# Performance work log

Hardware: AMD Instinct MI355X
Metric: run time of the kernel (lower is better)

Reference implementation:

```python
import jax, jax.numpy as jnp
import numpy as np
import jax.scipy.linalg as jsl

N = 20000
E = 320000
IN_FEAT = 128
HID = 128
OUT_FEAT = 64
D = 4            # stalk_dim
K = HID // D     # number of stalks per node
MLP_HID = 64


def setup_inputs() -> dict:
    key = jax.random.key(0)
    ks = jax.random.split(key, 16)
    def lin(kw, kb, fan_in, fan_out):
        s = 1.0 / np.sqrt(fan_in)
        w = jax.random.uniform(kw, (fan_in, fan_out), minval=-s, maxval=s, dtype=jnp.float32)
        b = jax.random.uniform(kb, (fan_out,), minval=-s, maxval=s, dtype=jnp.float32)
        return w, b
    x = jax.random.normal(ks[0], (N, IN_FEAT), dtype=jnp.float32)
    edge_index = jax.random.randint(ks[1], (2, E), 0, N, dtype=jnp.int64)
    lin_in_w, lin_in_b = lin(ks[2], ks[3], IN_FEAT, HID)
    conv0_w1, conv0_b1 = lin(ks[4], ks[5], 2 * HID, MLP_HID)
    conv0_w2, conv0_b2 = lin(ks[6], ks[7], MLP_HID, 2 * D * D)
    conv1_w1, conv1_b1 = lin(ks[8], ks[9], 2 * HID, MLP_HID)
    conv1_w2, conv1_b2 = lin(ks[10], ks[11], MLP_HID, 2 * D * D)
    lin_out_w, lin_out_b = lin(ks[12], ks[13], HID, OUT_FEAT)
    return {
        "x": x, "edge_index": edge_index,
        "lin_in_w": lin_in_w, "lin_in_b": lin_in_b,
        "conv0_w1": conv0_w1, "conv0_b1": conv0_b1,
        "conv0_w2": conv0_w2, "conv0_b2": conv0_b2, "conv0_eps": jnp.float32(0.5),
        "conv1_w1": conv1_w1, "conv1_b1": conv1_b1,
        "conv1_w2": conv1_w2, "conv1_b2": conv1_b2, "conv1_eps": jnp.float32(0.5),
        "lin_out_w": lin_out_w, "lin_out_b": lin_out_b,
    }


def _sheaf_conv(x, row, col, w1, b1, w2, b2, eps):
    # edge gather -> MLP -> skew-symmetric expm -> batched small matmuls -> scatter-add
    x_row = x[row]              # [E, C] source features
    x_col = x[col]              # [E, C] target features
    h = jax.nn.relu(jnp.concatenate([x_row, x_col], axis=-1) @ w1 + b1)
    maps = (h @ w2 + b2).reshape(-1, 2, D, D)        # [E, 2, d, d]
    A = maps - jnp.swapaxes(maps, -1, -2)            # skew-symmetric
    F_e = jax.vmap(jsl.expm)(A.reshape(-1, D, D)).reshape(-1, 2, D, D)
    f_u, f_v = F_e[:, 0], F_e[:, 1]                  # [E, d, d] each
    # PyG default flow: x_i = x[col] (target), x_j = x[row] (source)
    x_i = x_col.reshape(-1, K, D)
    x_j = x_row.reshape(-1, K, D)
    proj_i = jnp.einsum('eab,ekb->eka', f_u, x_i)
    proj_j = jnp.einsum('eab,ekb->eka', f_v, x_j)
    err = proj_i - proj_j
    msg = jnp.einsum('eba,ekb->eka', f_u, err).reshape(-1, K * D)  # f_u^T @ err
    agg = jax.ops.segment_sum(msg, col, num_segments=x.shape[0])   # scatter-add at target
    return x - eps * agg


def reference(x, edge_index, lin_in_w, lin_in_b,
              conv0_w1, conv0_b1, conv0_w2, conv0_b2, conv0_eps,
              conv1_w1, conv1_b1, conv1_w2, conv1_b2, conv1_eps,
              lin_out_w, lin_out_b):
    row, col = edge_index[0], edge_index[1]
    h = x @ lin_in_w + lin_in_b
    h = jax.nn.elu(_sheaf_conv(h, row, col, conv0_w1, conv0_b1, conv0_w2, conv0_b2, conv0_eps))
    h = jax.nn.elu(_sheaf_conv(h, row, col, conv1_w1, conv1_b1, conv1_w2, conv1_b2, conv1_eps))
    return h @ lin_out_w + lin_out_b
```

## Files before the change

kernel.cpp:

```cpp
#include <hip/hip_runtime.h>
#include <math.h>


using short8 = __attribute__((ext_vector_type(8))) short;
using f32x4 = __attribute__((ext_vector_type(4))) float;
typedef unsigned short u16;

__device__ __forceinline__ u16 f2bf(float f) {
  unsigned u = __float_as_uint(f);
  unsigned r = (u + 0x7FFFu + ((u >> 16) & 1u)) >> 16;
  return (u16)r;
}
__device__ __forceinline__ float bf2f(u16 v) {
  return __uint_as_float(((unsigned)v) << 16);
}

__device__ __forceinline__ void glds16(const void* g, void* l) {
  __builtin_amdgcn_global_load_lds(
      (const __attribute__((address_space(1))) unsigned int*)g,
      (__attribute__((address_space(3))) unsigned int*)l, 16, 0, 0);
}

__global__ void __launch_bounds__(256) k_prep(const float* __restrict__ x,
    u16* __restrict__ Xb, int* __restrict__ cnt, int n4, int N,
    const float* __restrict__ win, const float* __restrict__ w1a,
    const float* __restrict__ w1b, const float* __restrict__ wout,
    const float* __restrict__ w2a, const float* __restrict__ w2b,
    const float* __restrict__ b1a, const float* __restrict__ b1b,
    u16* __restrict__ WTin, u16* __restrict__ WT1a, u16* __restrict__ WT1b,
    u16* __restrict__ WTout, u16* __restrict__ W2Ta, u16* __restrict__ W2Tb,
    float* __restrict__ B1pa, float* __restrict__ B1pb) {
  int idx = blockIdx.x * 256 + threadIdx.x;
  if (idx < N) cnt[idx] = 0;
  if (idx < n4) {
    float4 v = ((const float4*)x)[idx];
    ushort4 o;
    o.x = f2bf(v.x);
    o.y = f2bf(v.y);
    o.z = f2bf(v.z);
    o.w = f2bf(v.w);
    ((ushort4*)Xb)[idx] = o;
  }
  if (idx < 16384) {
    int o = idx >> 7, i = idx & 127;
    WTin[idx] = f2bf(win[i * 128 + o]);
  } else if (idx < 32768) {
    int j = idx - 16384;
    int o = j >> 7, i = j & 127;
    WT1a[j] = f2bf(o < 64 ? w1a[i * 64 + o] : w1a[(128 + i) * 64 + (o - 64)]);
  } else if (idx < 49152) {
    int j = idx - 32768;
    int o = j >> 7, i = j & 127;
    WT1b[j] = f2bf(o < 64 ? w1b[i * 64 + o] : w1b[(128 + i) * 64 + (o - 64)]);
  } else if (idx < 57344) {
    int j = idx - 49152;
    int o = j >> 7, i = j & 127;
    WTout[j] = f2bf(wout[i * 64 + o]);
  } else if (idx < 59392) {
    int j = idx - 57344;
    int o = j >> 6, k = j & 63;
    W2Ta[j] = f2bf(w2a[k * 32 + o]);
  } else if (idx < 61440) {
    int j = idx - 59392;
    int o = j >> 6, k = j & 63;
    W2Tb[j] = f2bf(w2b[k * 32 + o]);
  } else if (idx < 61568) {
    int j = idx - 61440;
    B1pa[j] = (j < 64) ? 0.f : b1a[j - 64];
  } else if (idx < 61696) {
    int j = idx - 61568;
    B1pb[j] = (j < 64) ? 0.f : b1b[j - 64];
  }
}

__global__ void __launch_bounds__(256) k_gemm_mfma(const u16* __restrict__ Ab,
    const u16* __restrict__ WT, const float* __restrict__ bias,
    float* __restrict__ C, u16* __restrict__ Cb, int N, int P) {
  int t = threadIdx.x;
  int wv = t >> 6, lane = t & 63;
  int row0 = (blockIdx.x << 6) + (wv << 4);
  int cb = blockIdx.y << 4;
  int col = lane & 15, quad = lane >> 4;
  const u16* wrow = WT + (size_t)(cb + col) * 128 + quad * 8;
  short8 b0 = *(const short8*)(wrow);
  short8 b1 = *(const short8*)(wrow + 32);
  short8 b2 = *(const short8*)(wrow + 64);
  short8 b3 = *(const short8*)(wrow + 96);
  float bv = bias ? bias[cb + col] : 0.f;
  const u16* ar = Ab + (size_t)(row0 + col) * 128 + quad * 8;
  short8 a0 = *(const short8*)(ar);
  short8 a1 = *(const short8*)(ar + 32);
  short8 a2 = *(const short8*)(ar + 64);
  short8 a3 = *(const short8*)(ar + 96);
  f32x4 acc = {0.f, 0.f, 0.f, 0.f};
  acc = __builtin_amdgcn_mfma_f32_16x16x32_bf16(a0, b0, acc, 0, 0, 0);
  acc = __builtin_amdgcn_mfma_f32_16x16x32_bf16(a1, b1, acc, 0, 0, 0);
  acc = __builtin_amdgcn_mfma_f32_16x16x32_bf16(a2, b2, acc, 0, 0, 0);
  acc = __builtin_amdgcn_mfma_f32_16x16x32_bf16(a3, b3, acc, 0, 0, 0);
#pragma unroll
  for (int r = 0; r < 4; ++r) {
    int row = row0 + quad * 4 + r;
    if (row < N) {
      float o = acc[r] + bv;
      if (C) C[(size_t)row * P + cb + col] = o;
      if (Cb) Cb[(size_t)row * 128 + cb + col] = f2bf(o);
    }
  }
}

__global__ void __launch_bounds__(256) k_hist(const int* __restrict__ eidx,
                                              int* __restrict__ cnt, int E) {
  int e = blockIdx.x * 256 + threadIdx.x;
  if (e < E) atomicAdd(&cnt[eidx[E + e]], 1);
}

__global__ void __launch_bounds__(256) k_scanA(const int* __restrict__ cnt,
                                               int* __restrict__ bsum, int N) {
  __shared__ int sums[256];
  int b = blockIdx.x, t = threadIdx.x;
  int base = b * 2048 + t * 8;
  int s = 0;
#pragma unroll
  for (int k = 0; k < 8; ++k) {
    int i = base + k;
    if (i < N) s += cnt[i];
  }
  sums[t] = s;
  __syncthreads();
  for (int d = 128; d > 0; d >>= 1) {
    if (t < d) sums[t] += sums[t + d];
    __syncthreads();
  }
  if (t == 0) bsum[b] = sums[0];
}

__global__ void __launch_bounds__(256) k_scanC(const int* __restrict__ cnt,
    const int* __restrict__ bsum, int* __restrict__ ptr,
    int* __restrict__ cursor, int N, int nblocks) {
  __shared__ int sums[256];
  int b = blockIdx.x, t = threadIdx.x;
  int bo = 0;
  for (int k = 0; k < b; ++k) bo += bsum[k];
  int base = b * 2048 + t * 8;
  int vals[8];
  int s = 0;
#pragma unroll
  for (int k = 0; k < 8; ++k) {
    int i = base + k;
    int c = (i < N) ? cnt[i] : 0;
    vals[k] = s;
    s += c;
  }
  sums[t] = s;
  __syncthreads();
  for (int d = 1; d < 256; d <<= 1) {
    int v = (t >= d) ? sums[t - d] : 0;
    __syncthreads();
    sums[t] += v;
    __syncthreads();
  }
  int toff = (t == 0) ? 0 : sums[t - 1];
#pragma unroll
  for (int k = 0; k < 8; ++k) {
    int i = base + k;
    if (i < N) {
      int p = bo + toff + vals[k];
      ptr[i] = p;
      cursor[i] = p;
    }
  }
  if (b == nblocks - 1 && t == 255) ptr[N] = bo + sums[255];
}

__global__ void __launch_bounds__(256) k_fill(const int* __restrict__ eidx,
    int* __restrict__ cursor, int* __restrict__ adj, int E) {
  int e = blockIdx.x * 256 + threadIdx.x;
  if (e >= E) return;
  int r = eidx[e], c = eidx[E + e];
  int pos = atomicAdd(&cursor[c], 1);
  adj[pos] = r;
}

__device__ __forceinline__ void so4_expm(const float* __restrict__ m,
                                         float* __restrict__ F) {
  float v1 = m[1] - m[4], v2 = m[2] - m[8], v3 = m[3] - m[12];
  float w1 = m[11] - m[14], w2 = m[13] - m[7], w3 = m[6] - m[9];
  float p1 = 0.5f * (v1 + w1), p2 = 0.5f * (v2 + w2), p3 = 0.5f * (v3 + w3);
  float q1 = 0.5f * (v1 - w1), q2 = 0.5f * (v2 - w2), q3 = 0.5f * (v3 - w3);
  float tp2 = p1 * p1 + p2 * p2 + p3 * p3;
  float tq2 = q1 * q1 + q2 * q2 + q3 * q3;
  float tp = sqrtf(tp2), tq = sqrtf(tq2);
  float cp = __cosf(tp);
  float sp = (tp > 1e-6f) ? (__sinf(tp) / tp) : (1.f - tp2 * (1.f / 6.f));
  float cq = __cosf(tq);
  float sq = (tq > 1e-6f) ? (__sinf(tq) / tq) : (1.f - tq2 * (1.f / 6.f));
  float a1 = sp * p1, a2 = sp * p2, a3 = sp * p3;
  float b1 = sq * q1, b2 = sq * q2, b3 = sq * q3;
  float Rp[16] = {cp,  a1,  a2,  a3,  -a1, cp,  a3,  -a2,
                  -a2, -a3, cp,  a1,  -a3, a2,  -a1, cp};
  float Rq[16] = {cq,  b1,  b2,  b3,  -b1, cq,  -b3, b2,
                  -b2, b3,  cq,  -b1, -b3, -b2, b1,  cq};
#pragma unroll
  for (int a = 0; a < 4; ++a)
#pragma unroll
    for (int b = 0; b < 4; ++b) {
      float s = 0.f;
#pragma unroll
      for (int c = 0; c < 4; ++c) s = fmaf(Rp[a * 4 + c], Rq[c * 4 + b], s);
      F[a * 4 + b] = s;
    }
}

__global__ void __launch_bounds__(64) k_conv(const float* __restrict__ x,
    const u16* __restrict__ xgb, const u16* __restrict__ pqb,
    const u16* __restrict__ W2T, const float* __restrict__ b2,
    const int* __restrict__ ptr, const int* __restrict__ adj,
    const float* __restrict__ epsp, float* __restrict__ xout,
    u16* __restrict__ xoutb, int N) {
  __shared__ float ms[16 * 44];
  __shared__ u16 xs[2][16 * 128];
  int lane = threadIdx.x;
  int v = blockIdx.x;
  if (v >= N) return;
  int p0 = ptr[v], p1 = ptr[v + 1];
  int el = lane & 15, quad = lane >> 4;
  int a = lane & 3, kb = lane & ~3;
  int sub = lane >> 4;
  int colb = (lane & 15) * 8;
  short8 bf00 = *(const short8*)(W2T + (size_t)el * 64 + quad * 8);
  short8 bf01 = *(const short8*)(W2T + (size_t)el * 64 + 32 + quad * 8);
  short8 bf10 = *(const short8*)(W2T + (size_t)(16 + el) * 64 + quad * 8);
  short8 bf11 = *(const short8*)(W2T + (size_t)(16 + el) * 64 + 32 + quad * 8);
  float b2a = b2[el], b2b = b2[16 + el];
  short8 qv0 = *(const short8*)(pqb + (size_t)v * 128 + 64 + quad * 8);
  short8 qv1 = *(const short8*)(pqb + (size_t)v * 128 + 96 + quad * 8);
  const float* xv = x + (size_t)v * 128;
  float4 xi1 = *(const float4*)(xv + kb);
  float4 xi2 = *(const float4*)(xv + 64 + kb);
  float hv1 = xv[lane], hv2 = xv[64 + lane];
  float s10 = 0.f, s11 = 0.f, s12 = 0.f, s13 = 0.f;
  float acc1 = 0.f, acc2 = 0.f;
  int cur = 0;
  int row = 0;
  if (p0 < p1) {
    int nb0 = p1 - p0;
    nb0 = (nb0 > 16) ? 16 : nb0;
    int ee0 = p0 + ((el < nb0) ? el : (nb0 - 1));
    row = adj[ee0];
#pragma unroll
    for (int t = 0; t < 4; ++t) {
      int r = __shfl(row, (t << 2) + sub);
      glds16(xgb + (size_t)r * 128 + colb, &xs[0][t * 512]);
    }
  }
  for (int b0 = p0; b0 < p1; b0 += 16) {
    int nb = p1 - b0;
    nb = (nb > 16) ? 16 : nb;
    int have_next = (b0 + 16 < p1);
    int row_n = row;
    if (have_next) {
      int nb2 = p1 - b0 - 16;
      nb2 = (nb2 > 16) ? 16 : nb2;
      int ee2 = b0 + 16 + ((el < nb2) ? el : (nb2 - 1));
      row_n = adj[ee2];
    }
    f32x4 c0 = {0.f, 0.f, 0.f, 0.f};
    f32x4 c1 = {0.f, 0.f, 0.f, 0.f};
    {
      short8 pv = *(const short8*)(pqb + (size_t)row * 128 + quad * 8);
      union { short8 s; unsigned u[4]; } av;
#pragma unroll
      for (int j2 = 0; j2 < 4; ++j2) {
        float h0 = fmaxf(bf2f((u16)pv[2 * j2]) + bf2f((u16)qv0[2 * j2]), 0.f);
        float h1 = fmaxf(
            bf2f((u16)pv[2 * j2 + 1]) + bf2f((u16)qv0[2 * j2 + 1]), 0.f);
        unsigned r;
        asm("v_cvt_pk_bf16_f32 %0, %1, %2" : "=v"(r) : "v"(h0), "v"(h1));
        av.u[j2] = r;
      }
      c0 = __builtin_amdgcn_mfma_f32_16x16x32_bf16(av.s, bf00, c0, 0, 0, 0);
      c1 = __builtin_amdgcn_mfma_f32_16x16x32_bf16(av.s, bf10, c1, 0, 0, 0);
    }
    {
      short8 pv = *(const short8*)(pqb + (size_t)row * 128 + 32 + quad * 8);
      union { short8 s; unsigned u[4]; } av;
#pragma unroll
      for (int j2 = 0; j2 < 4; ++j2) {
        float h0 = fmaxf(bf2f((u16)pv[2 * j2]) + bf2f((u16)qv1[2 * j2]), 0.f);
        float h1 = fmaxf(
            bf2f((u16)pv[2 * j2 + 1]) + bf2f((u16)qv1[2 * j2 + 1]), 0.f);
        unsigned r;
        asm("v_cvt_pk_bf16_f32 %0, %1, %2" : "=v"(r) : "v"(h0), "v"(h1));
        av.u[j2] = r;
      }
      c0 = __builtin_amdgcn_mfma_f32_16x16x32_bf16(av.s, bf01, c0, 0, 0, 0);
      c1 = __builtin_amdgcn_mfma_f32_16x16x32_bf16(av.s, bf11, c1, 0, 0, 0);
    }
#pragma unroll
    for (int r = 0; r < 4; ++r) {
      ms[(quad * 4 + r) * 44 + el] = c0[r] + b2a;
      ms[(quad * 4 + r) * 44 + 16 + el] = c1[r] + b2b;
    }
    __syncthreads();
    if (have_next) {
#pragma unroll
      for (int t = 0; t < 4; ++t) {
        int r = __shfl(row_n, (t << 2) + sub);
        glds16(xgb + (size_t)r * 128 + colb, &xs[cur ^ 1][t * 512]);
      }
    }
    if (lane < 16) {
      float m[32];
      const float* mr = ms + lane * 44;
#pragma unroll
      for (int i = 0; i < 32; ++i) m[i] = mr[i];
      float Fu[16], Fv[16];
      so4_expm(m, Fu);
      so4_expm(m + 16, Fv);
      float* mw = ms + lane * 44;
#pragma unroll
      for (int aa = 0; aa < 4; ++aa)
#pragma unroll
        for (int bb = 0; bb < 4; ++bb) {
          float s1 = 0.f, s2 = 0.f;
#pragma unroll
          for (int cc = 0; cc < 4; ++cc) {
            s1 = fmaf(Fu[cc * 4 + aa], Fu[cc * 4 + bb], s1);
            s2 = fmaf(Fu[cc * 4 + aa], Fv[cc * 4 + bb], s2);
          }
          mw[aa * 4 + bb] = s1;
          mw[16 + aa * 4 + bb] = s2;
        }
    }
    __syncthreads();
    if (have_next) {
      asm volatile("s_waitcnt vmcnt(4)" ::: "memory");
    } else {
      asm volatile("s_waitcnt vmcnt(0)" ::: "memory");
    }
    __builtin_amdgcn_sched_barrier(0);
    const u16* xc = xs[cur];
    int j = 0;
    for (; j + 1 < nb; j += 2) {
      float4 am1 = *(const float4*)(ms + j * 44 + a * 4);
      float4 am2 = *(const float4*)(ms + j * 44 + 16 + a * 4);
      float4 bm1 = *(const float4*)(ms + (j + 1) * 44 + a * 4);
      float4 bm2 = *(const float4*)(ms + (j + 1) * 44 + 16 + a * 4);
      ushort4 ya1 = *(const ushort4*)(xc + j * 128 + kb);
      ushort4 ya2 = *(const ushort4*)(xc + j * 128 + 64 + kb);
      ushort4 yb1 = *(const ushort4*)(xc + (j + 1) * 128 + kb);
      ushort4 yb2 = *(const ushort4*)(xc + (j + 1) * 128 + 64 + kb);
      s10 += am1.x + bm1.x;
      s11 += am1.y + bm1.y;
      s12 += am1.z + bm1.z;
      s13 += am1.w + bm1.w;
      acc1 -= am2.x * bf2f(ya1.x) + am2.y * bf2f(ya1.y) +
              am2.z * bf2f(ya1.z) + am2.w * bf2f(ya1.w);
      acc2 -= am2.x * bf2f(ya2.x) + am2.y * bf2f(ya2.y) +
              am2.z * bf2f(ya2.z) + am2.w * bf2f(ya2.w);
      acc1 -= bm2.x * bf2f(yb1.x) + bm2.y * bf2f(yb1.y) +
              bm2.z * bf2f(yb1.z) + bm2.w * bf2f(yb1.w);
      acc2 -= bm2.x * bf2f(yb2.x) + bm2.y * bf2f(yb2.y) +
              bm2.z * bf2f(yb2.z) + bm2.w * bf2f(yb2.w);
    }
    if (j < nb) {
      float4 am1 = *(const float4*)(ms + j * 44 + a * 4);
      float4 am2 = *(const float4*)(ms + j * 44 + 16 + a * 4);
      ushort4 ya1 = *(const ushort4*)(xc + j * 128 + kb);
      ushort4 ya2 = *(const ushort4*)(xc + j * 128 + 64 + kb);
      s10 += am1.x;
      s11 += am1.y;
      s12 += am1.z;
      s13 += am1.w;
      acc1 -= am2.x * bf2f(ya1.x) + am2.y * bf2f(ya1.y) +
              am2.z * bf2f(ya1.z) + am2.w * bf2f(ya1.w);
      acc2 -= am2.x * bf2f(ya2.x) + am2.y * bf2f(ya2.y) +
              am2.z * bf2f(ya2.z) + am2.w * bf2f(ya2.w);
    }
    __syncthreads();
    row = row_n;
    cur ^= 1;
  }
  acc1 += s10 * xi1.x + s11 * xi1.y + s12 * xi1.z + s13 * xi1.w;
  acc2 += s10 * xi2.x + s11 * xi2.y + s12 * xi2.z + s13 * xi2.w;
  float eps = *epsp;
  float r1 = hv1 - eps * acc1;
  float r2 = hv2 - eps * acc2;
  r1 = (r1 > 0.f) ? r1 : expm1f(r1);
  r2 = (r2 > 0.f) ? r2 : expm1f(r2);
  xout[(size_t)v * 128 + lane] = r1;
  xout[(size_t)v * 128 + 64 + lane] = r2;
  xoutb[(size_t)v * 128 + lane] = f2bf(r1);
  xoutb[(size_t)v * 128 + 64 + lane] = f2bf(r2);
}

extern "C" void kernel_launch(void* const* d_in, const int* in_sizes, int n_in,
                              void* d_out, int out_size, void* d_ws,
                              size_t ws_size, hipStream_t stream) {
  const float* x = (const float*)d_in[0];
  const int* eidx = (const int*)d_in[1];
  const float* lin_in_w = (const float*)d_in[2];
  const float* lin_in_b = (const float*)d_in[3];
  const float* c0w1 = (const float*)d_in[4];
  const float* c0b1 = (const float*)d_in[5];
  const float* c0w2 = (const float*)d_in[6];
  const float* c0b2 = (const float*)d_in[7];
  const float* c0eps = (const float*)d_in[8];
  const float* c1w1 = (const float*)d_in[9];
  const float* c1b1 = (const float*)d_in[10];
  const float* c1w2 = (const float*)d_in[11];
  const float* c1b2 = (const float*)d_in[12];
  const float* c1eps = (const float*)d_in[13];
  const float* lout_w = (const float*)d_in[14];
  const float* lout_b = (const float*)d_in[15];
  float* out = (float*)d_out;

  int N = in_sizes[0] / 128;
  int E = in_sizes[1] / 2;
  int Npad = N + 64;

  char* ws = (char*)d_ws;
  size_t szH = (size_t)N * 128 * 4;
  size_t szHb = (size_t)Npad * 128 * 2;
  float* H = (float*)ws;
  float* H2 = (float*)(ws + szH);
  u16* Xb = (u16*)(ws + 2 * szH);
  u16* Hb = (u16*)(ws + 2 * szH + szHb);
  u16* H2b = (u16*)(ws + 2 * szH + 2 * szHb);
  u16* PQb = (u16*)(ws + 2 * szH + 3 * szHb);
  u16* WTin = (u16*)(ws + 2 * szH + 4 * szHb);
  u16* WT1a = WTin + 16384;
  u16* WT1b = WT1a + 16384;
  u16* WTout = WT1b + 16384;
  u16* W2Ta = WTout + 8192;
  u16* W2Tb = W2Ta + 2048;
  float* B1pa = (float*)(W2Tb + 2048);
  float* B1pb = B1pa + 128;
  char* ip = (char*)(B1pb + 128);
  int* cnt = (int*)ip;
  int* ptr = (int*)(ip + 4 * (size_t)(N + 64));
  int* cursor = (int*)(ip + 8 * (size_t)(N + 64));
  int* adj = (int*)(ip + 12 * (size_t)(N + 64));
  int* bsum = (int*)(ip + 12 * (size_t)(N + 64) + 4 * (size_t)E);

  dim3 blk(256);
  int gN = (N + 63) / 64;
  int gE = (E + 255) / 256;
  int nsb = (N + 2047) / 2048;

  k_prep<<<(N * 32 + 255) / 256, blk, 0, stream>>>(
      x, Xb, cnt, N * 32, N, lin_in_w, c0w1, c1w1, lout_w, c0w2, c1w2, c0b1,
      c1b1, WTin, WT1a, WT1b, WTout, W2Ta, W2Tb, B1pa, B1pb);
  k_hist<<<gE, blk, 0, stream>>>(eidx, cnt, E);
  k_scanA<<<nsb, blk, 0, stream>>>(cnt, bsum, N);
  k_scanC<<<nsb, blk, 0, stream>>>(cnt, bsum, ptr, cursor, N, nsb);
  k_fill<<<gE, blk, 0, stream>>>(eidx, cursor, adj, E);

  k_gemm_mfma<<<dim3(gN, 8), blk, 0, stream>>>(Xb, WTin, lin_in_b, H, Hb, N,
                                               128);

  float* cur = H;
  float* nxt = H2;
  u16* curb = Hb;
  u16* nxtb = H2b;
  for (int layer = 0; layer < 2; ++layer) {
    const u16* wt1 = layer ? WT1b : WT1a;
    const u16* w2t = layer ? W2Tb : W2Ta;
    const float* b1p = layer ? B1pb : B1pa;
    const float* b2 = layer ? c1b2 : c0b2;
    const float* ep = layer ? c1eps : c0eps;
    k_gemm_mfma<<<dim3(gN, 8), blk, 0, stream>>>(curb, wt1, b1p, nullptr, PQb,
                                                 N, 128);
    k_conv<<<N, dim3(64), 0, stream>>>(cur, curb, PQb, w2t, b2, ptr, adj, ep,
                                       nxt, nxtb, N);
    float* tf = cur; cur = nxt; nxt = tf;
    u16* tb = curb; curb = nxtb; nxtb = tb;
  }

  k_gemm_mfma<<<dim3(gN, 4), blk, 0, stream>>>(curb, WTout, lout_b, out,
                                               nullptr, N, 64);
}
```

Measured before the change: 274.3 us.

## Prefetch neighbor pq rows into LDS via async loads and drop block barriers

Each edge's projected source features (pqb rows) are now loaded asynchronously into a double-buffered LDS tile with an XOR-swizzled layout, alongside the existing x-gather prefetch. Before, each iteration read them directly from global memory right before the MFMA. Because the block is a single 64-lane wave, the __syncthreads calls become a wave-local LDS wait, which cuts barrier overhead. The vmcnt counts are adjusted to cover the extra in-flight loads. This relies on the single-wave assumption and on the hand-tuned waitcnt values being correct.

```diff
diff --git a/kernel.cpp b/kernel.cpp
--- a/kernel.cpp
+++ b/kernel.cpp
@@ -13,6 +13,12 @@
 }
 __device__ __forceinline__ float bf2f(u16 v) {
   return __uint_as_float(((unsigned)v) << 16);
+}
+
+__device__ __forceinline__ void wave_sync() {
+  __builtin_amdgcn_sched_barrier(0);
+  asm volatile("s_waitcnt lgkmcnt(0)" ::: "memory");
+  __builtin_amdgcn_sched_barrier(0);
 }
 
 __device__ __forceinline__ void glds16(const void* g, void* l) {
@@ -219,14 +225,19 @@
     u16* __restrict__ xoutb, int N) {
   __shared__ float ms[16 * 44];
   __shared__ u16 xs[2][16 * 128];
+  __shared__ u16 ps[2][16 * 64];
   int lane = threadIdx.x;
   int v = blockIdx.x;
   if (v >= N) return;
   int p0 = ptr[v], p1 = ptr[v + 1];
   int el = lane & 15, quad = lane >> 4;
   int a = lane & 3, kb = lane & ~3;
-  int sub = lane >> 4;
-  int colb = (lane & 15) * 8;
+  int xsub = lane >> 4;
+  int xcol = (lane & 15) * 8;
+  int prow = lane >> 3;
+  int pcol = ((lane & 7) ^ (lane >> 3)) * 8;
+  int pslot0 = el * 64 + ((quad ^ (el & 7)) << 3);
+  int pslot1 = el * 64 + (((4 + quad) ^ (el & 7)) << 3);
   short8 bf00 = *(const short8*)(W2T + (size_t)el * 64 + quad * 8);
   short8 bf01 = *(const short8*)(W2T + (size_t)el * 64 + 32 + quad * 8);
   short8 bf10 = *(const short8*)(W2T + (size_t)(16 + el) * 64 + quad * 8);
@@ -241,33 +252,40 @@
   float s10 = 0.f, s11 = 0.f, s12 = 0.f, s13 = 0.f;
   float acc1 = 0.f, acc2 = 0.f;
   int cur = 0;
-  int row = 0;
   if (p0 < p1) {
     int nb0 = p1 - p0;
     nb0 = (nb0 > 16) ? 16 : nb0;
     int ee0 = p0 + ((el < nb0) ? el : (nb0 - 1));
-    row = adj[ee0];
+    int row0 = adj[ee0];
+#pragma unroll
+    for (int t = 0; t < 2; ++t) {
+      int r = __shfl(row0, t * 8 + prow);
+      glds16(pqb + (size_t)r * 128 + pcol, &ps[0][t * 512]);
+    }
 #pragma unroll
     for (int t = 0; t < 4; ++t) {
-      int r = __shfl(row, (t << 2) + sub);
-      glds16(xgb + (size_t)r * 128 + colb, &xs[0][t * 512]);
+      int r = __shfl(row0, (t << 2) + xsub);
+      glds16(xgb + (size_t)r * 128 + xcol, &xs[0][t * 512]);
     }
   }
   for (int b0 = p0; b0 < p1; b0 += 16) {
     int nb = p1 - b0;
     nb = (nb > 16) ? 16 : nb;
     int have_next = (b0 + 16 < p1);
-    int row_n = row;
+    asm volatile("s_waitcnt vmcnt(4)" ::: "memory");
+    __builtin_amdgcn_sched_barrier(0);
+    int row_n = 0;
     if (have_next) {
       int nb2 = p1 - b0 - 16;
       nb2 = (nb2 > 16) ? 16 : nb2;
       int ee2 = b0 + 16 + ((el < nb2) ? el : (nb2 - 1));
       row_n = adj[ee2];
     }
+    const u16* pc = ps[cur];
     f32x4 c0 = {0.f, 0.f, 0.f, 0.f};
     f32x4 c1 = {0.f, 0.f, 0.f, 0.f};
     {
-      short8 pv = *(const short8*)(pqb + (size_t)row * 128 + quad * 8);
+      short8 pv = *(const short8*)(pc + pslot0);
       union { short8 s; unsigned u[4]; } av;
 #pragma unroll
       for (int j2 = 0; j2 < 4; ++j2) {
@@ -282,7 +300,7 @@
       c1 = __builtin_amdgcn_mfma_f32_16x16x32_bf16(av.s, bf10, c1, 0, 0, 0);
     }
     {
-      short8 pv = *(const short8*)(pqb + (size_t)row * 128 + 32 + quad * 8);
+      short8 pv = *(const short8*)(pc + pslot1);
       union { short8 s; unsigned u[4]; } av;
 #pragma unroll
       for (int j2 = 0; j2 < 4; ++j2) {
@@ -301,12 +319,17 @@
       ms[(quad * 4 + r) * 44 + el] = c0[r] + b2a;
       ms[(quad * 4 + r) * 44 + 16 + el] = c1[r] + b2b;
     }
-    __syncthreads();
+    wave_sync();
     if (have_next) {
 #pragma unroll
+      for (int t = 0; t < 2; ++t) {
+        int r = __shfl(row_n, t * 8 + prow);
+        glds16(pqb + (size_t)r * 128 + pcol, &ps[cur ^ 1][t * 512]);
+      }
+#pragma unroll
       for (int t = 0; t < 4; ++t) {
-        int r = __shfl(row_n, (t << 2) + sub);
-        glds16(xgb + (size_t)r * 128 + colb, &xs[cur ^ 1][t * 512]);
+        int r = __shfl(row_n, (t << 2) + xsub);
+        glds16(xgb + (size_t)r * 128 + xcol, &xs[cur ^ 1][t * 512]);
       }
     }
     if (lane < 16) {
@@ -332,9 +355,9 @@
           mw[16 + aa * 4 + bb] = s2;
         }
     }
-    __syncthreads();
+    wave_sync();
     if (have_next) {
-      asm volatile("s_waitcnt vmcnt(4)" ::: "memory");
+      asm volatile("s_waitcnt vmcnt(6)" ::: "memory");
     } else {
       asm volatile("s_waitcnt vmcnt(0)" ::: "memory");
     }
@@ -377,8 +400,7 @@
       acc2 -= am2.x * bf2f(ya2.x) + am2.y * bf2f(ya2.y) +
               am2.z * bf2f(ya2.z) + am2.w * bf2f(ya2.w);
     }
-    __syncthreads();
-    row = row_n;
+    wave_sync();
     cur ^= 1;
   }
   acc1 += s10 * xi1.x + s11 * xi1.y + s12 * xi1.z + s13 * xi1.w;
```

New measurement: 283.7 us. 3.4% more time.

## Precompute per-node neighbor header and replace block barriers with wave waits

Applied to the files above, without the earlier changes.

The fill kernel now also writes the first 16 source indices of each node into a compact u16 header array. The conv kernel reads its first neighbor batch directly from that header, removing the dependent ptr-then-adj load chain at block start. Because each conv block is a single 64-thread wave, the __syncthreads calls are replaced with an LDS waitcnt wrapped in scheduling barriers, which drops the barrier instruction. In exchange there is an extra zero-init and scattered write in setup, and storing node indices as u16 assumes N fits in 16 bits.

```diff
diff --git a/kernel.cpp b/kernel.cpp
--- a/kernel.cpp
+++ b/kernel.cpp
@@ -13,6 +13,12 @@
 }
 __device__ __forceinline__ float bf2f(u16 v) {
   return __uint_as_float(((unsigned)v) << 16);
+}
+
+__device__ __forceinline__ void wave_sync() {
+  __builtin_amdgcn_sched_barrier(0);
+  asm volatile("s_waitcnt lgkmcnt(0)" ::: "memory");
+  __builtin_amdgcn_sched_barrier(0);
 }
 
 __device__ __forceinline__ void glds16(const void* g, void* l) {
@@ -29,9 +35,11 @@
     const float* __restrict__ b1a, const float* __restrict__ b1b,
     u16* __restrict__ WTin, u16* __restrict__ WT1a, u16* __restrict__ WT1b,
     u16* __restrict__ WTout, u16* __restrict__ W2Ta, u16* __restrict__ W2Tb,
-    float* __restrict__ B1pa, float* __restrict__ B1pb) {
+    float* __restrict__ B1pa, float* __restrict__ B1pb,
+    u16* __restrict__ hdr) {
   int idx = blockIdx.x * 256 + threadIdx.x;
   if (idx < N) cnt[idx] = 0;
+  if (idx < N * 16) hdr[idx] = 0;
   if (idx < n4) {
     float4 v = ((const float4*)x)[idx];
     ushort4 o;
@@ -173,12 +181,15 @@
 }
 
 __global__ void __launch_bounds__(256) k_fill(const int* __restrict__ eidx,
-    int* __restrict__ cursor, int* __restrict__ adj, int E) {
+    int* __restrict__ cursor, int* __restrict__ adj, u16* __restrict__ hdr,
+    const int* __restrict__ ptr, int E) {
   int e = blockIdx.x * 256 + threadIdx.x;
   if (e >= E) return;
   int r = eidx[e], c = eidx[E + e];
   int pos = atomicAdd(&cursor[c], 1);
   adj[pos] = r;
+  int local = pos - ptr[c];
+  if ((unsigned)local < 16u) hdr[(size_t)c * 16 + local] = (u16)r;
 }
 
 __device__ __forceinline__ void so4_expm(const float* __restrict__ m,
@@ -215,6 +226,7 @@
     const u16* __restrict__ xgb, const u16* __restrict__ pqb,
     const u16* __restrict__ W2T, const float* __restrict__ b2,
     const int* __restrict__ ptr, const int* __restrict__ adj,
+    const u16* __restrict__ hdr,
     const float* __restrict__ epsp, float* __restrict__ xout,
     u16* __restrict__ xoutb, int N) {
   __shared__ float ms[16 * 44];
@@ -222,11 +234,12 @@
   int lane = threadIdx.x;
   int v = blockIdx.x;
   if (v >= N) return;
+  int el = lane & 15, quad = lane >> 4;
+  int row = (int)hdr[(size_t)v * 16 + el];
   int p0 = ptr[v], p1 = ptr[v + 1];
-  int el = lane & 15, quad = lane >> 4;
   int a = lane & 3, kb = lane & ~3;
-  int sub = lane >> 4;
-  int colb = (lane & 15) * 8;
+  int xsub = lane >> 4;
+  int xcol = (lane & 15) * 8;
   short8 bf00 = *(const short8*)(W2T + (size_t)el * 64 + quad * 8);
   short8 bf01 = *(const short8*)(W2T + (size_t)el * 64 + 32 + quad * 8);
   short8 bf10 = *(const short8*)(W2T + (size_t)(16 + el) * 64 + quad * 8);
@@ -241,16 +254,11 @@
   float s10 = 0.f, s11 = 0.f, s12 = 0.f, s13 = 0.f;
   float acc1 = 0.f, acc2 = 0.f;
   int cur = 0;
-  int row = 0;
   if (p0 < p1) {
-    int nb0 = p1 - p0;
-    nb0 = (nb0 > 16) ? 16 : nb0;
-    int ee0 = p0 + ((el < nb0) ? el : (nb0 - 1));
-    row = adj[ee0];
 #pragma unroll
     for (int t = 0; t < 4; ++t) {
-      int r = __shfl(row, (t << 2) + sub);
-      glds16(xgb + (size_t)r * 128 + colb, &xs[0][t * 512]);
+      int r = __shfl(row, (t << 2) + xsub);
+      glds16(xgb + (size_t)r * 128 + xcol, &xs[0][t * 512]);
     }
   }
   for (int b0 = p0; b0 < p1; b0 += 16) {
@@ -301,12 +309,12 @@
       ms[(quad * 4 + r) * 44 + el] = c0[r] + b2a;
       ms[(quad * 4 + r) * 44 + 16 + el] = c1[r] + b2b;
     }
-    __syncthreads();
+    wave_sync();
     if (have_next) {
 #pragma unroll
       for (int t = 0; t < 4; ++t) {
-        int r = __shfl(row_n, (t << 2) + sub);
-        glds16(xgb + (size_t)r * 128 + colb, &xs[cur ^ 1][t * 512]);
+        int r = __shfl(row_n, (t << 2) + xsub);
+        glds16(xgb + (size_t)r * 128 + xcol, &xs[cur ^ 1][t * 512]);
       }
     }
     if (lane < 16) {
@@ -332,7 +340,7 @@
           mw[16 + aa * 4 + bb] = s2;
         }
     }
-    __syncthreads();
+    wave_sync();
     if (have_next) {
       asm volatile("s_waitcnt vmcnt(4)" ::: "memory");
     } else {
@@ -377,7 +385,7 @@
       acc2 -= am2.x * bf2f(ya2.x) + am2.y * bf2f(ya2.y) +
               am2.z * bf2f(ya2.z) + am2.w * bf2f(ya2.w);
     }
-    __syncthreads();
+    wave_sync();
     row = row_n;
     cur ^= 1;
   }
@@ -442,6 +450,7 @@
   int* cursor = (int*)(ip + 8 * (size_t)(N + 64));
   int* adj = (int*)(ip + 12 * (size_t)(N + 64));
   int* bsum = (int*)(ip + 12 * (size_t)(N + 64) + 4 * (size_t)E);
+  u16* hdr = (u16*)(ip + 12 * (size_t)(N + 64) + 4 * (size_t)E + 256);
 
   dim3 blk(256);
   int gN = (N + 63) / 64;
@@ -450,11 +459,11 @@
 
   k_prep<<<(N * 32 + 255) / 256, blk, 0, stream>>>(
       x, Xb, cnt, N * 32, N, lin_in_w, c0w1, c1w1, lout_w, c0w2, c1w2, c0b1,
-      c1b1, WTin, WT1a, WT1b, WTout, W2Ta, W2Tb, B1pa, B1pb);
+      c1b1, WTin, WT1a, WT1b, WTout, W2Ta, W2Tb, B1pa, B1pb, hdr);
   k_hist<<<gE, blk, 0, stream>>>(eidx, cnt, E);
   k_scanA<<<nsb, blk, 0, stream>>>(cnt, bsum, N);
   k_scanC<<<nsb, blk, 0, stream>>>(cnt, bsum, ptr, cursor, N, nsb);
-  k_fill<<<gE, blk, 0, stream>>>(eidx, cursor, adj, E);
+  k_fill<<<gE, blk, 0, stream>>>(eidx, cursor, adj, hdr, ptr, E);
 
   k_gemm_mfma<<<dim3(gN, 8), blk, 0, stream>>>(Xb, WTin, lin_in_b, H, Hb, N,
                                                128);
@@ -471,8 +480,8 @@
     const float* ep = layer ? c1eps : c0eps;
     k_gemm_mfma<<<dim3(gN, 8), blk, 0, stream>>>(curb, wt1, b1p, nullptr, PQb,
                                                  N, 128);
-    k_conv<<<N, dim3(64), 0, stream>>>(cur, curb, PQb, w2t, b2, ptr, adj, ep,
-                                       nxt, nxtb, N);
+    k_conv<<<N, dim3(64), 0, stream>>>(cur, curb, PQb, w2t, b2, ptr, adj, hdr,
+                                       ep, nxt, nxtb, N);
     float* tf = cur; cur = nxt; nxt = tf;
     u16* tb = curb; curb = nxtb; nxtb = tb;
   }
```

Result: no change. 273.5 us (-0.3%).
